# Performance work log

Measured on AMD Instinct MI355X. Metric: run time of the kernel, lower is better.

The kernel has to match this reference:

```python
import jax, jax.numpy as jnp
import numpy as np

EPS = 1e-8


def decode_fcos_obb(loc, deltas):
    """FCOS-style OBB decode. deltas = (d_x-, d_y-, d_z-, d_x+, d_y+, d_z+, theta):
    distances from the point to the 6 box faces, measured in the box's yaw-rotated
    frame. Returns OBB (x, y, z, w, l, h, theta)."""
    theta = deltas[:, 6]
    w = deltas[:, 0] + deltas[:, 3]
    l = deltas[:, 1] + deltas[:, 4]
    h = deltas[:, 2] + deltas[:, 5]
    ox = (deltas[:, 3] - deltas[:, 0]) * 0.5
    oy = (deltas[:, 4] - deltas[:, 1]) * 0.5
    oz = (deltas[:, 5] - deltas[:, 2]) * 0.5
    c, s = jnp.cos(theta), jnp.sin(theta)
    cx = loc[:, 0] + ox * c - oy * s
    cy = loc[:, 1] + ox * s + oy * c
    cz = loc[:, 2] + oz
    return jnp.stack([cx, cy, cz, w, l, h, theta], axis=-1)


def box2corners(box):
    # box: (B,N,5) = (x,y,w,h,alpha) -> (B,N,4,2) CCW corners
    x, y, w, h, a = (box[..., i] for i in range(5))
    x4 = jnp.asarray([0.5, -0.5, -0.5, 0.5], box.dtype) * w[..., None]
    y4 = jnp.asarray([0.5, 0.5, -0.5, -0.5], box.dtype) * h[..., None]
    c, s = jnp.cos(a)[..., None], jnp.sin(a)[..., None]
    return jnp.stack([x4 * c - y4 * s + x[..., None],
                      x4 * s + y4 * c + y[..., None]], axis=-1)


def box_intersection(corners1, corners2):
    # Pairwise intersections of the 4 edges of box1 with the 4 edges of box2.
    # Returns points (B,N,4,4,2) and validity mask (B,N,4,4).
    l1 = jnp.concatenate([corners1, jnp.roll(corners1, -1, axis=2)], axis=-1)[:, :, :, None, :]
    l2 = jnp.concatenate([corners2, jnp.roll(corners2, -1, axis=2)], axis=-1)[:, :, None, :, :]
    x1, y1, x2, y2 = l1[..., 0], l1[..., 1], l1[..., 2], l1[..., 3]
    x3, y3, x4, y4 = l2[..., 0], l2[..., 1], l2[..., 2], l2[..., 3]
    num = (y4 - y3) * (x2 - x1) - (x4 - x3) * (y2 - y1)
    den_t = (x4 - x3) * (y1 - y3) - (y4 - y3) * (x1 - x3)
    den_u = (x2 - x1) * (y1 - y3) - (y2 - y1) * (x1 - x3)
    safe = jnp.where(num == 0., 1., num)
    t = jnp.where(num == 0., -1., den_t / safe)
    u = jnp.where(num == 0., -1., -den_u / safe)
    mask = (t > 0.) & (t < 1.) & (u > 0.) & (u < 1.)
    t2 = den_t / (num + EPS)
    pts = jnp.stack([x1 + t2 * (x2 - x1), y1 + t2 * (y2 - y1)], axis=-1)
    pts = pts * mask[..., None].astype(pts.dtype)
    return pts, mask


def box1_in_box2(corners1, corners2):
    # Which corners of box1 lie inside box2 (projection onto box2's edge frame).
    a = corners2[:, :, 0:1, :]
    b = corners2[:, :, 1:2, :]
    d = corners2[:, :, 3:4, :]
    ab, ad, am = b - a, d - a, corners1 - a
    p_ab = (ab * am).sum(-1) / (ab * ab).sum(-1)
    p_ad = (ad * am).sum(-1) / (ad * ad).sum(-1)
    tol = 1e-6
    return (p_ab > -tol) & (p_ab < 1 + tol) & (p_ad > -tol) & (p_ad < 1 + tol)


def sorted_polygon_area(vertices, mask):
    # vertices: (B,N,24,2) candidate polygon vertices, mask: (B,N,24) validity.
    # Sort valid vertices CCW around their centroid, pad with the first vertex,
    # shoelace area. Equivalent to Rotated_IoU's sort_vertices + calculate_area.
    m = mask.astype(vertices.dtype)
    nv = m.sum(-1)  # (B,N) number of valid vertices
    mean = (vertices * m[..., None]).sum(2) / jnp.maximum(nv, 1.)[..., None]
    v = vertices - mean[:, :, None, :]
    ang = jnp.where(mask, jnp.arctan2(v[..., 1], v[..., 0]), 1e6)  # invalid -> last
    idx = jnp.argsort(ang, axis=-1)
    vs = jnp.take_along_axis(v, idx[..., None], axis=2)
    pos = jnp.arange(vertices.shape[2])
    pad = pos[None, None, :] >= nv[..., None]
    vs = jnp.where(pad[..., None], vs[:, :, :1, :], vs)  # pad with first valid vertex
    nxt = jnp.roll(vs, -1, axis=2)
    cross = vs[..., 0] * nxt[..., 1] - vs[..., 1] * nxt[..., 0]
    return 0.5 * jnp.abs(cross.sum(-1))


def cal_iou(box1, box2):
    c1 = box2corners(box1)
    c2 = box2corners(box2)
    pts, m_i = box_intersection(c1, c2)
    B, N = box1.shape[:2]
    vertices = jnp.concatenate([c1, c2, pts.reshape(B, N, 16, 2)], axis=2)
    mask = jnp.concatenate([box1_in_box2(c1, c2), box1_in_box2(c2, c1),
                            m_i.reshape(B, N, 16)], axis=2)
    inter = sorted_polygon_area(vertices, mask)
    u = box1[..., 2] * box1[..., 3] + box2[..., 2] * box2[..., 3] - inter
    return inter / u, u


def cal_iou_3d(b1, b2):
    # boxes: (B,N,7) = (x,y,z,w,l,h,theta); 2D rotated IoU in xy, overlap in z.
    box1 = jnp.stack([b1[..., 0], b1[..., 1], b1[..., 3], b1[..., 4], b1[..., 6]], -1)
    box2 = jnp.stack([b2[..., 0], b2[..., 1], b2[..., 3], b2[..., 4], b2[..., 6]], -1)
    zmax1, zmin1 = b1[..., 2] + b1[..., 5] * 0.5, b1[..., 2] - b1[..., 5] * 0.5
    zmax2, zmin2 = b2[..., 2] + b2[..., 5] * 0.5, b2[..., 2] - b2[..., 5] * 0.5
    z_overlap = jnp.clip(jnp.minimum(zmax1, zmax2) - jnp.maximum(zmin1, zmin2), 0.)
    iou_2d, u = cal_iou(box1, box2)
    inter_3d = iou_2d * u * z_overlap
    v1 = b1[..., 3] * b1[..., 4] * b1[..., 5]
    v2 = b2[..., 3] * b2[..., 4] * b2[..., 5]
    u3d = v1 + v2 - inter_3d
    return inter_3d / u3d, u3d


def rotated_iou_loss(pred, target, weight):
    loc = jnp.zeros((pred.shape[0], 3), pred.dtype)
    pb = decode_fcos_obb(loc, pred)[None]     # (1,N,7)
    tb = decode_fcos_obb(loc, target)[None]   # (1,N,7)
    ious, unions = cal_iou_3d(pb, tb)
    vol_inter = ious * unions
    ious = (vol_inter + 1.0) / (unions + 1.0)  # smoothed IoU
    losses = -jnp.log(ious)
    return (losses * weight).sum()


def setup_inputs():
    key = jax.random.key(0)
    k1, k2, k3 = jax.random.split(key, 3)
    N = 250000

    def make_deltas(k):
        u = jax.random.uniform(k, (N, 7), dtype=jnp.float32)
        dists = u[:, :6] * 2.0 + 0.3               # positive face distances
        theta = (u[:, 6:7] - 0.5) * jnp.pi          # yaw in (-pi/2, pi/2)
        return jnp.concatenate([dists, theta], axis=1)

    return {
        "pred": make_deltas(k1),
        "target": make_deltas(k2),
        "weight": jax.random.uniform(k3, (N,), dtype=jnp.float32),
    }


def reference(pred, target, weight):
    return rotated_iou_loss(pred, target, weight)
```

## Files before the change

kernel.cpp:

```cpp
#include <hip/hip_runtime.h>
#include <math.h>


#define RCP(x) __builtin_amdgcn_rcpf(x)

__global__ __launch_bounds__(256, 2) void riou_loss_kernel(
    const float* __restrict__ pred, const float* __restrict__ tgt,
    const float* __restrict__ wgt, float* __restrict__ ws, int n)
{
    int i = blockIdx.x * 256 + threadIdx.x;
    float loss = 0.0f;
    if (i < n) {
        const float* pp = pred + 7 * i;
        const float* qq = tgt + 7 * i;
        float p0 = pp[0], p1 = pp[1], p2 = pp[2], p3 = pp[3], p4 = pp[4], p5 = pp[5], p6 = pp[6];
        float q0 = qq[0], q1 = qq[1], q2 = qq[2], q3 = qq[3], q4 = qq[4], q5 = qq[5], q6 = qq[6];

        float w1 = p0 + p3, l1 = p1 + p4, h1 = p2 + p5;
        float oz1 = (p5 - p2) * 0.5f;
        float ox1 = (p3 - p0) * 0.5f, oy1 = (p4 - p1) * 0.5f;
        float sA = __sinf(p6), cA = __cosf(p6);
        float cx1 = ox1 * cA - oy1 * sA, cy1 = ox1 * sA + oy1 * cA;

        float w2 = q0 + q3, l2 = q1 + q4, h2 = q2 + q5;
        float oz2 = (q5 - q2) * 0.5f;
        float ox2 = (q3 - q0) * 0.5f, oy2 = (q4 - q1) * 0.5f;
        float sB = __sinf(q6), cB = __cosf(q6);
        float cx2 = ox2 * cB - oy2 * sB, cy2 = ox2 * sB + oy2 * cB;

        float vol1 = w1 * l1 * h1, vol2 = w2 * l2 * h2;
        float zo = fmaxf(fminf(oz1 + h1 * 0.5f, oz2 + h2 * 0.5f) -
                         fmaxf(oz1 - h1 * 0.5f, oz2 - h2 * 0.5f), 0.0f);

        float hw1 = 0.5f * w1, hl1 = 0.5f * l1;
        float c1x0 =  hw1 * cA - hl1 * sA + cx1, c1y0 =  hw1 * sA + hl1 * cA + cy1;
        float c1x1 = -hw1 * cA - hl1 * sA + cx1, c1y1 = -hw1 * sA + hl1 * cA + cy1;
        float c1x2 = -hw1 * cA + hl1 * sA + cx1, c1y2 = -hw1 * sA - hl1 * cA + cy1;
        float c1x3 =  hw1 * cA + hl1 * sA + cx1, c1y3 =  hw1 * sA - hl1 * cA + cy1;
        float hw2 = 0.5f * w2, hl2 = 0.5f * l2;
        float c2x0 =  hw2 * cB - hl2 * sB + cx2, c2y0 =  hw2 * sB + hl2 * cB + cy2;
        float c2x1 = -hw2 * cB - hl2 * sB + cx2, c2y1 = -hw2 * sB + hl2 * cB + cy2;
        float c2x2 = -hw2 * cB + hl2 * sB + cx2, c2y2 = -hw2 * sB - hl2 * cB + cy2;
        float c2x3 =  hw2 * cB + hl2 * sB + cx2, c2y3 =  hw2 * sB - hl2 * cB + cy2;

        float sumx = 0.0f, sumy = 0.0f;
        int nv = 0;
#define ACC(M, X, Y) { sumx += (M) ? (X) : 0.0f; sumy += (M) ? (Y) : 0.0f; nv += (M) ? 1 : 0; }

        const float TOL = 1e-6f;
        float abxB = c2x1 - c2x0, abyB = c2y1 - c2y0;
        float adxB = c2x3 - c2x0, adyB = c2y3 - c2y0;
        float rabB = RCP(abxB * abxB + abyB * abyB);
        float radB = RCP(adxB * adxB + adyB * adyB);
#define PIB_B(MX, MY, M) { float amx = (MX) - c2x0, amy = (MY) - c2y0; \
        float pab = (abxB * amx + abyB * amy) * rabB; \
        float pdd = (adxB * amx + adyB * amy) * radB; \
        M = (pab > -TOL) & (pab < 1.0f + TOL) & (pdd > -TOL) & (pdd < 1.0f + TOL); }
        bool mA0, mA1, mA2, mA3;
        PIB_B(c1x0, c1y0, mA0) PIB_B(c1x1, c1y1, mA1)
        PIB_B(c1x2, c1y2, mA2) PIB_B(c1x3, c1y3, mA3)
        ACC(mA0, c1x0, c1y0) ACC(mA1, c1x1, c1y1) ACC(mA2, c1x2, c1y2) ACC(mA3, c1x3, c1y3)
        float abxA = c1x1 - c1x0, abyA = c1y1 - c1y0;
        float adxA = c1x3 - c1x0, adyA = c1y3 - c1y0;
        float rabA = RCP(abxA * abxA + abyA * abyA);
        float radA = RCP(adxA * adxA + adyA * adyA);
#define PIB_A(MX, MY, M) { float amx = (MX) - c1x0, amy = (MY) - c1y0; \
        float pab = (abxA * amx + abyA * amy) * rabA; \
        float pdd = (adxA * amx + adyA * amy) * radA; \
        M = (pab > -TOL) & (pab < 1.0f + TOL) & (pdd > -TOL) & (pdd < 1.0f + TOL); }
        bool mB0, mB1, mB2, mB3;
        PIB_A(c2x0, c2y0, mB0) PIB_A(c2x1, c2y1, mB1)
        PIB_A(c2x2, c2y2, mB2) PIB_A(c2x3, c2y3, mB3)
        ACC(mB0, c2x0, c2y0) ACC(mB1, c2x1, c2y1) ACC(mB2, c2x2, c2y2) ACC(mB3, c2x3, c2y3)

#define ISECT(X1, Y1, X2, Y2, X3, Y3, X4, Y4, PX, PY, M) { \
        float ex = (X2) - (X1), ey = (Y2) - (Y1); \
        float fx = (X4) - (X3), fy = (Y4) - (Y3); \
        float gx = (X1) - (X3), gy = (Y1) - (Y3); \
        float num = fy * ex - fx * ey; \
        float dt_ = fx * gy - fy * gx; \
        float du_ = ex * gy - ey * gx; \
        float rr = RCP(num); \
        float tt = dt_ * rr, uu = -du_ * rr; \
        M = (tt > 0.0f) & (tt < 1.0f) & (uu > 0.0f) & (uu < 1.0f); \
        PX = (X1) + tt * ex; PY = (Y1) + tt * ey; }
#define SITEM(PX, PY, M, OX0, OY0, OX1, OY1, CNT) { \
        bool tk0 = (M) && ((CNT) == 0); bool tk1 = (M) && ((CNT) == 1); \
        OX0 = tk0 ? (PX) : OX0; OY0 = tk0 ? (PY) : OY0; \
        OX1 = tk1 ? (PX) : OX1; OY1 = tk1 ? (PY) : OY1; \
        CNT += (M) ? 1 : 0; }
#define EDGE_GROUP(X1, Y1, X2, Y2, EX0, EY0, EX1, EY1) { \
        int gc = 0; float px, py; bool mm; \
        ISECT(X1, Y1, X2, Y2, c2x0, c2y0, c2x1, c2y1, px, py, mm) \
        ACC(mm, px, py) SITEM(px, py, mm, EX0, EY0, EX1, EY1, gc) \
        ISECT(X1, Y1, X2, Y2, c2x1, c2y1, c2x2, c2y2, px, py, mm) \
        ACC(mm, px, py) SITEM(px, py, mm, EX0, EY0, EX1, EY1, gc) \
        ISECT(X1, Y1, X2, Y2, c2x2, c2y2, c2x3, c2y3, px, py, mm) \
        ACC(mm, px, py) SITEM(px, py, mm, EX0, EY0, EX1, EY1, gc) \
        ISECT(X1, Y1, X2, Y2, c2x3, c2y3, c2x0, c2y0, px, py, mm) \
        ACC(mm, px, py) SITEM(px, py, mm, EX0, EY0, EX1, EY1, gc) }

        float vx8 = 0.f, vy8 = 0.f, vx9 = 0.f, vy9 = 0.f;
        float vx10 = 0.f, vy10 = 0.f, vx11 = 0.f, vy11 = 0.f;
        float vx12 = 0.f, vy12 = 0.f, vx13 = 0.f, vy13 = 0.f;
        float vx14 = 0.f, vy14 = 0.f, vx15 = 0.f, vy15 = 0.f;
        int nv8_before = nv;
        EDGE_GROUP(c1x0, c1y0, c1x1, c1y1, vx8, vy8, vx9, vy9)
        int nv10_before = nv;
        EDGE_GROUP(c1x1, c1y1, c1x2, c1y2, vx10, vy10, vx11, vy11)
        int nv12_before = nv;
        EDGE_GROUP(c1x2, c1y2, c1x3, c1y3, vx12, vy12, vx13, vy13)
        int nv14_before = nv;
        EDGE_GROUP(c1x3, c1y3, c1x0, c1y0, vx14, vy14, vx15, vy15)
        bool m8  = (nv10_before - nv8_before) > 0, m9  = (nv10_before - nv8_before) > 1;
        bool m10 = (nv12_before - nv10_before) > 0, m11 = (nv12_before - nv10_before) > 1;
        bool m12 = (nv14_before - nv12_before) > 0, m13 = (nv14_before - nv12_before) > 1;
        bool m14 = (nv - nv14_before) > 0,          m15 = (nv - nv14_before) > 1;

        float vx0 = c1x0, vy0 = c1y0, vx1 = c1x1, vy1 = c1y1;
        float vx2 = c1x2, vy2 = c1y2, vx3 = c1x3, vy3 = c1y3;
        float vx4 = c2x0, vy4 = c2y0, vx5 = c2x1, vy5 = c2y1;
        float vx6 = c2x2, vy6 = c2y2, vx7 = c2x3, vy7 = c2y3;
        bool m0 = mA0, m1 = mA1, m2 = mA2, m3 = mA3;
        bool m4 = mB0, m5 = mB1, m6 = mB2, m7 = mB3;

        float inv_nv = RCP(fmaxf((float)nv, 1.0f));
        float mx_ = sumx * inv_nv, my_ = sumy * inv_nv;
        float ang0, ang1, ang2, ang3, ang4, ang5, ang6, ang7;
        float ang8, ang9, ang10, ang11, ang12, ang13, ang14, ang15;
        unsigned pk0, pk1, pk2, pk3, pk4, pk5, pk6, pk7;
        unsigned pk8, pk9, pk10, pk11, pk12, pk13, pk14, pk15;
#define ANGPACK(K) { float xc = vx##K - mx_, yc = vy##K - my_; \
        float dd = yc * RCP(fmaxf(fabsf(xc) + fabsf(yc), 1e-38f)); \
        ang##K = m##K ? ((xc >= 0.0f) ? dd : copysignf(2.0f, yc) - dd) : 1e6f; \
        pk##K = (__float_as_uint(xc) & 0xFFFF0000u) | (__float_as_uint(yc) >> 16); }
        ANGPACK(0) ANGPACK(1) ANGPACK(2) ANGPACK(3)
        ANGPACK(4) ANGPACK(5) ANGPACK(6) ANGPACK(7)
        ANGPACK(8) ANGPACK(9) ANGPACK(10) ANGPACK(11)
        ANGPACK(12) ANGPACK(13) ANGPACK(14) ANGPACK(15)

#define CE(A, B) { bool sw = ang##A > ang##B; \
        float mn = fminf(ang##A, ang##B), mx2 = fmaxf(ang##A, ang##B); \
        ang##A = mn; ang##B = mx2; \
        unsigned ta = pk##A; pk##A = sw ? pk##B : pk##A; pk##B = sw ? ta : pk##B; }
        CE(0,1) CE(2,3) CE(4,5) CE(6,7) CE(8,9) CE(10,11) CE(12,13) CE(14,15)
        CE(0,2) CE(1,3) CE(4,6) CE(5,7) CE(8,10) CE(9,11) CE(12,14) CE(13,15)
        CE(1,2) CE(5,6) CE(9,10) CE(13,14)
        CE(0,4) CE(1,5) CE(2,6) CE(3,7) CE(8,12) CE(9,13) CE(10,14) CE(11,15)
        CE(2,4) CE(3,5) CE(10,12) CE(11,13)
        CE(1,2) CE(3,4) CE(5,6) CE(9,10) CE(11,12) CE(13,14)
        CE(0,8) CE(1,9) CE(2,10) CE(3,11) CE(4,12) CE(5,13) CE(6,14) CE(7,15)
        CE(4,8) CE(5,9) CE(6,10) CE(7,11)
        CE(2,4) CE(3,5) CE(6,8) CE(7,9) CE(10,12) CE(11,13)
        CE(1,2) CE(3,4) CE(5,6) CE(7,8) CE(9,10) CE(11,12) CE(13,14)

#define PAD(K) { pk##K = (ang##K > 5e5f) ? pk0 : pk##K; }
        PAD(1) PAD(2) PAD(3) PAD(4) PAD(5) PAD(6) PAD(7) PAD(8)
        PAD(9) PAD(10) PAD(11) PAD(12) PAD(13) PAD(14) PAD(15)

#define UPX(K) float ux##K = __uint_as_float(pk##K & 0xFFFF0000u); \
               float uy##K = __uint_as_float(pk##K << 16);
        UPX(0) UPX(1) UPX(2) UPX(3) UPX(4) UPX(5) UPX(6) UPX(7)
        UPX(8) UPX(9) UPX(10) UPX(11) UPX(12) UPX(13) UPX(14) UPX(15)
        float cs = 0.0f;
#define SHOE(A, B) cs += ux##A * uy##B - uy##A * ux##B;
        SHOE(0,1) SHOE(1,2) SHOE(2,3) SHOE(3,4) SHOE(4,5) SHOE(5,6) SHOE(6,7) SHOE(7,8)
        SHOE(8,9) SHOE(9,10) SHOE(10,11) SHOE(11,12) SHOE(12,13) SHOE(13,14) SHOE(14,15) SHOE(15,0)
        float inter = 0.5f * fabsf(cs);

        float inter3d = inter * zo;
        float u3d = vol1 + vol2 - inter3d;
        float iouf = (inter3d + 1.0f) * RCP(u3d + 1.0f);
        loss = -__logf(iouf) * wgt[i];
    }

#pragma unroll
    for (int off = 32; off > 0; off >>= 1)
        loss += __shfl_down(loss, off, 64);
    __shared__ float wsum[4];
    int lane = threadIdx.x & 63, wid = threadIdx.x >> 6;
    if (lane == 0) wsum[wid] = loss;
    __syncthreads();
    if (threadIdx.x == 0)
        ws[blockIdx.x] = wsum[0] + wsum[1] + wsum[2] + wsum[3];
}

__global__ __launch_bounds__(256) void riou_reduce_kernel(
    const float* __restrict__ ws, float* __restrict__ out, int nb)
{
    float s = 0.0f;
    for (int t = threadIdx.x; t < nb; t += 256) s += ws[t];
#pragma unroll
    for (int off = 32; off > 0; off >>= 1)
        s += __shfl_down(s, off, 64);
    __shared__ float wsum[4];
    int lane = threadIdx.x & 63, wid = threadIdx.x >> 6;
    if (lane == 0) wsum[wid] = s;
    __syncthreads();
    if (threadIdx.x == 0)
        out[0] = wsum[0] + wsum[1] + wsum[2] + wsum[3];
}

extern "C" void kernel_launch(void* const* d_in, const int* in_sizes, int n_in,
                              void* d_out, int out_size, void* d_ws, size_t ws_size,
                              hipStream_t stream) {
    const float* pred = (const float*)d_in[0];
    const float* tgt  = (const float*)d_in[1];
    const float* wgt  = (const float*)d_in[2];
    float* out = (float*)d_out;
    float* ws  = (float*)d_ws;
    int n = in_sizes[2];

    int block = 256;
    int grid = (n + block - 1) / block;
    riou_loss_kernel<<<grid, block, 0, stream>>>(pred, tgt, wgt, ws, n);
    riou_reduce_kernel<<<1, block, 0, stream>>>(ws, out, grid);
}
```

Before: 77.06 us.

## Process two boxes per thread with paired float2-style arithmetic

Each thread now handles two elements (t and t+256) using a small f2 struct so the compiler can emit packed FP32 (v_pk_*) instructions on CDNA, and the grid is halved. Range checks are rewritten as |x-0.5|<0.5 forms, and the angle key uses a different pseudo-angle formula. Out-of-range elements are clamped and weighted by zero rather than branched. The risk is higher register pressure from doubled live state, which under launch_bounds(256,2) could cause spills or lower occupancy.

```diff
diff --git a/kernel.cpp b/kernel.cpp
--- a/kernel.cpp
+++ b/kernel.cpp
@@ -3,94 +3,139 @@
 
 
 #define RCP(x) __builtin_amdgcn_rcpf(x)
+
+struct f2 { float a, b; };
+struct b2 { bool a, b; };
+struct i2 { int a, b; };
+struct u2 { unsigned a, b; };
+
+__device__ __forceinline__ f2 operator+(f2 p, f2 q) { return {p.a + q.a, p.b + q.b}; }
+__device__ __forceinline__ f2 operator-(f2 p, f2 q) { return {p.a - q.a, p.b - q.b}; }
+__device__ __forceinline__ f2 operator*(f2 p, f2 q) { return {p.a * q.a, p.b * q.b}; }
+__device__ __forceinline__ f2 operator*(float s, f2 q) { return {s * q.a, s * q.b}; }
+__device__ __forceinline__ f2 operator-(f2 p) { return {-p.a, -p.b}; }
+__device__ __forceinline__ f2 rcp2(f2 p) { return {RCP(p.a), RCP(p.b)}; }
+__device__ __forceinline__ f2 fmin2(f2 p, f2 q) { return {fminf(p.a, q.a), fminf(p.b, q.b)}; }
+__device__ __forceinline__ f2 fmax2(f2 p, f2 q) { return {fmaxf(p.a, q.a), fmaxf(p.b, q.b)}; }
+__device__ __forceinline__ f2 fabs2(f2 p) { return {fabsf(p.a), fabsf(p.b)}; }
+__device__ __forceinline__ f2 cps2(f2 p, f2 s) { return {copysignf(p.a, s.a), copysignf(p.b, s.b)}; }
+__device__ __forceinline__ f2 sin2(f2 p) { return {__sinf(p.a), __sinf(p.b)}; }
+__device__ __forceinline__ f2 cos2(f2 p) { return {__cosf(p.a), __cosf(p.b)}; }
+__device__ __forceinline__ f2 log2f2(f2 p) { return {__logf(p.a), __logf(p.b)}; }
+__device__ __forceinline__ b2 lt2(f2 p, f2 q) { return {p.a < q.a, p.b < q.b}; }
+__device__ __forceinline__ b2 gt2(f2 p, f2 q) { return {p.a > q.a, p.b > q.b}; }
+__device__ __forceinline__ b2 and2(b2 p, b2 q) { return {p.a && q.a, p.b && q.b}; }
+__device__ __forceinline__ f2 sel(b2 c, f2 p, f2 q) { return {c.a ? p.a : q.a, c.b ? p.b : q.b}; }
+__device__ __forceinline__ u2 selu(b2 c, u2 p, u2 q) { return {c.a ? p.a : q.a, c.b ? p.b : q.b}; }
+__device__ __forceinline__ f2 i2f(i2 p) { return {(float)p.a, (float)p.b}; }
+
+__device__ __forceinline__ u2 pack2(f2 x, f2 y) {
+    return {(__float_as_uint(x.a) & 0xFFFF0000u) | (__float_as_uint(y.a) >> 16),
+            (__float_as_uint(x.b) & 0xFFFF0000u) | (__float_as_uint(y.b) >> 16)};
+}
+__device__ __forceinline__ f2 unpx(u2 p) {
+    return {__uint_as_float(p.a & 0xFFFF0000u), __uint_as_float(p.b & 0xFFFF0000u)};
+}
+__device__ __forceinline__ f2 unpy(u2 p) {
+    return {__uint_as_float(p.a << 16), __uint_as_float(p.b << 16)};
+}
 
 __global__ __launch_bounds__(256, 2) void riou_loss_kernel(
     const float* __restrict__ pred, const float* __restrict__ tgt,
     const float* __restrict__ wgt, float* __restrict__ ws, int n)
 {
-    int i = blockIdx.x * 256 + threadIdx.x;
-    float loss = 0.0f;
-    if (i < n) {
-        const float* pp = pred + 7 * i;
-        const float* qq = tgt + 7 * i;
-        float p0 = pp[0], p1 = pp[1], p2 = pp[2], p3 = pp[3], p4 = pp[4], p5 = pp[5], p6 = pp[6];
-        float q0 = qq[0], q1 = qq[1], q2 = qq[2], q3 = qq[3], q4 = qq[4], q5 = qq[5], q6 = qq[6];
-
-        float w1 = p0 + p3, l1 = p1 + p4, h1 = p2 + p5;
-        float oz1 = (p5 - p2) * 0.5f;
-        float ox1 = (p3 - p0) * 0.5f, oy1 = (p4 - p1) * 0.5f;
-        float sA = __sinf(p6), cA = __cosf(p6);
-        float cx1 = ox1 * cA - oy1 * sA, cy1 = ox1 * sA + oy1 * cA;
-
-        float w2 = q0 + q3, l2 = q1 + q4, h2 = q2 + q5;
-        float oz2 = (q5 - q2) * 0.5f;
-        float ox2 = (q3 - q0) * 0.5f, oy2 = (q4 - q1) * 0.5f;
-        float sB = __sinf(q6), cB = __cosf(q6);
-        float cx2 = ox2 * cB - oy2 * sB, cy2 = ox2 * sB + oy2 * cB;
-
-        float vol1 = w1 * l1 * h1, vol2 = w2 * l2 * h2;
-        float zo = fmaxf(fminf(oz1 + h1 * 0.5f, oz2 + h2 * 0.5f) -
-                         fmaxf(oz1 - h1 * 0.5f, oz2 - h2 * 0.5f), 0.0f);
-
-        float hw1 = 0.5f * w1, hl1 = 0.5f * l1;
-        float c1x0 =  hw1 * cA - hl1 * sA + cx1, c1y0 =  hw1 * sA + hl1 * cA + cy1;
-        float c1x1 = -hw1 * cA - hl1 * sA + cx1, c1y1 = -hw1 * sA + hl1 * cA + cy1;
-        float c1x2 = -hw1 * cA + hl1 * sA + cx1, c1y2 = -hw1 * sA - hl1 * cA + cy1;
-        float c1x3 =  hw1 * cA + hl1 * sA + cx1, c1y3 =  hw1 * sA - hl1 * cA + cy1;
-        float hw2 = 0.5f * w2, hl2 = 0.5f * l2;
-        float c2x0 =  hw2 * cB - hl2 * sB + cx2, c2y0 =  hw2 * sB + hl2 * cB + cy2;
-        float c2x1 = -hw2 * cB - hl2 * sB + cx2, c2y1 = -hw2 * sB + hl2 * cB + cy2;
-        float c2x2 = -hw2 * cB + hl2 * sB + cx2, c2y2 = -hw2 * sB - hl2 * cB + cy2;
-        float c2x3 =  hw2 * cB + hl2 * sB + cx2, c2y3 =  hw2 * sB - hl2 * cB + cy2;
-
-        float sumx = 0.0f, sumy = 0.0f;
-        int nv = 0;
-#define ACC(M, X, Y) { sumx += (M) ? (X) : 0.0f; sumy += (M) ? (Y) : 0.0f; nv += (M) ? 1 : 0; }
-
-        const float TOL = 1e-6f;
-        float abxB = c2x1 - c2x0, abyB = c2y1 - c2y0;
-        float adxB = c2x3 - c2x0, adyB = c2y3 - c2y0;
-        float rabB = RCP(abxB * abxB + abyB * abyB);
-        float radB = RCP(adxB * adxB + adyB * adyB);
-#define PIB_B(MX, MY, M) { float amx = (MX) - c2x0, amy = (MY) - c2y0; \
-        float pab = (abxB * amx + abyB * amy) * rabB; \
-        float pdd = (adxB * amx + adyB * amy) * radB; \
-        M = (pab > -TOL) & (pab < 1.0f + TOL) & (pdd > -TOL) & (pdd < 1.0f + TOL); }
-        bool mA0, mA1, mA2, mA3;
-        PIB_B(c1x0, c1y0, mA0) PIB_B(c1x1, c1y1, mA1)
-        PIB_B(c1x2, c1y2, mA2) PIB_B(c1x3, c1y3, mA3)
-        ACC(mA0, c1x0, c1y0) ACC(mA1, c1x1, c1y1) ACC(mA2, c1x2, c1y2) ACC(mA3, c1x3, c1y3)
-        float abxA = c1x1 - c1x0, abyA = c1y1 - c1y0;
-        float adxA = c1x3 - c1x0, adyA = c1y3 - c1y0;
-        float rabA = RCP(abxA * abxA + abyA * abyA);
-        float radA = RCP(adxA * adxA + adyA * adyA);
-#define PIB_A(MX, MY, M) { float amx = (MX) - c1x0, amy = (MY) - c1y0; \
-        float pab = (abxA * amx + abyA * amy) * rabA; \
-        float pdd = (adxA * amx + adyA * amy) * radA; \
-        M = (pab > -TOL) & (pab < 1.0f + TOL) & (pdd > -TOL) & (pdd < 1.0f + TOL); }
-        bool mB0, mB1, mB2, mB3;
-        PIB_A(c2x0, c2y0, mB0) PIB_A(c2x1, c2y1, mB1)
-        PIB_A(c2x2, c2y2, mB2) PIB_A(c2x3, c2y3, mB3)
-        ACC(mB0, c2x0, c2y0) ACC(mB1, c2x1, c2y1) ACC(mB2, c2x2, c2y2) ACC(mB3, c2x3, c2y3)
+    const f2 zero = {0.f, 0.f}, half = {0.5f, 0.5f}, onev = {1.f, 1.f};
+    const f2 bigv = {1e6f, 1e6f}, big5 = {5e5f, 5e5f}, tiny = {1e-38f, 1e-38f};
+    const f2 htv = {0.5f + 1e-6f, 0.5f + 1e-6f};
+
+    int t0 = blockIdx.x * 512 + threadIdx.x;
+    int t1 = t0 + 256;
+    int ia = min(t0, n - 1), ib = min(t1, n - 1);
+    f2 wg = {(t0 < n) ? wgt[ia] : 0.0f, (t1 < n) ? wgt[ib] : 0.0f};
+
+    const float* pA = pred + 7 * ia;  const float* pB = pred + 7 * ib;
+    const float* qA = tgt + 7 * ia;   const float* qB = tgt + 7 * ib;
+    f2 p0 = {pA[0], pB[0]}, p1 = {pA[1], pB[1]}, p2 = {pA[2], pB[2]}, p3 = {pA[3], pB[3]};
+    f2 p4 = {pA[4], pB[4]}, p5 = {pA[5], pB[5]}, p6 = {pA[6], pB[6]};
+    f2 q0 = {qA[0], qB[0]}, q1 = {qA[1], qB[1]}, q2 = {qA[2], qB[2]}, q3 = {qA[3], qB[3]};
+    f2 q4 = {qA[4], qB[4]}, q5 = {qA[5], qB[5]}, q6 = {qA[6], qB[6]};
+
+    f2 w1 = p0 + p3, l1 = p1 + p4, h1 = p2 + p5;
+    f2 oz1 = 0.5f * (p5 - p2);
+    f2 ox1 = 0.5f * (p3 - p0), oy1 = 0.5f * (p4 - p1);
+    f2 sA = sin2(p6), cA = cos2(p6);
+    f2 cx1 = ox1 * cA - oy1 * sA, cy1 = ox1 * sA + oy1 * cA;
+
+    f2 w2 = q0 + q3, l2 = q1 + q4, h2 = q2 + q5;
+    f2 oz2 = 0.5f * (q5 - q2);
+    f2 ox2 = 0.5f * (q3 - q0), oy2 = 0.5f * (q4 - q1);
+    f2 sB = sin2(q6), cB = cos2(q6);
+    f2 cx2 = ox2 * cB - oy2 * sB, cy2 = ox2 * sB + oy2 * cB;
+
+    f2 vol1 = w1 * l1 * h1, vol2 = w2 * l2 * h2;
+    f2 zo = fmax2(fmin2(oz1 + 0.5f * h1, oz2 + 0.5f * h2) -
+                  fmax2(oz1 - 0.5f * h1, oz2 - 0.5f * h2), zero);
+
+    f2 hw1 = 0.5f * w1, hl1 = 0.5f * l1;
+    f2 c1x0 = hw1 * cA - hl1 * sA + cx1, c1y0 = hw1 * sA + hl1 * cA + cy1;
+    f2 c1x1 = zero - hw1 * cA - hl1 * sA + cx1, c1y1 = zero - hw1 * sA + hl1 * cA + cy1;
+    f2 c1x2 = zero - hw1 * cA + hl1 * sA + cx1, c1y2 = zero - hw1 * sA - hl1 * cA + cy1;
+    f2 c1x3 = hw1 * cA + hl1 * sA + cx1, c1y3 = hw1 * sA - hl1 * cA + cy1;
+    f2 hw2 = 0.5f * w2, hl2 = 0.5f * l2;
+    f2 c2x0 = hw2 * cB - hl2 * sB + cx2, c2y0 = hw2 * sB + hl2 * cB + cy2;
+    f2 c2x1 = zero - hw2 * cB - hl2 * sB + cx2, c2y1 = zero - hw2 * sB + hl2 * cB + cy2;
+    f2 c2x2 = zero - hw2 * cB + hl2 * sB + cx2, c2y2 = zero - hw2 * sB - hl2 * cB + cy2;
+    f2 c2x3 = hw2 * cB + hl2 * sB + cx2, c2y3 = hw2 * sB - hl2 * cB + cy2;
+
+    f2 sumx = zero, sumy = zero;
+    i2 nv = {0, 0};
+#define ACC(M, X, Y) { sumx = sumx + sel(M, X, zero); sumy = sumy + sel(M, Y, zero); \
+        nv.a += (M).a; nv.b += (M).b; }
+
+    f2 abxB = c2x1 - c2x0, abyB = c2y1 - c2y0;
+    f2 adxB = c2x3 - c2x0, adyB = c2y3 - c2y0;
+    f2 rabB = rcp2(abxB * abxB + abyB * abyB);
+    f2 radB = rcp2(adxB * adxB + adyB * adyB);
+#define PIB_B(MX, MY, M) { f2 amx = (MX) - c2x0, amy = (MY) - c2y0; \
+        f2 pab = (abxB * amx + abyB * amy) * rabB; \
+        f2 pdd = (adxB * amx + adyB * amy) * radB; \
+        M = and2(lt2(fabs2(pab - half), htv), lt2(fabs2(pdd - half), htv)); }
+    b2 mA0, mA1, mA2, mA3;
+    PIB_B(c1x0, c1y0, mA0) PIB_B(c1x1, c1y1, mA1)
+    PIB_B(c1x2, c1y2, mA2) PIB_B(c1x3, c1y3, mA3)
+    ACC(mA0, c1x0, c1y0) ACC(mA1, c1x1, c1y1) ACC(mA2, c1x2, c1y2) ACC(mA3, c1x3, c1y3)
+    f2 abxA = c1x1 - c1x0, abyA = c1y1 - c1y0;
+    f2 adxA = c1x3 - c1x0, adyA = c1y3 - c1y0;
+    f2 rabA = rcp2(abxA * abxA + abyA * abyA);
+    f2 radA = rcp2(adxA * adxA + adyA * adyA);
+#define PIB_A(MX, MY, M) { f2 amx = (MX) - c1x0, amy = (MY) - c1y0; \
+        f2 pab = (abxA * amx + abyA * amy) * rabA; \
+        f2 pdd = (adxA * amx + adyA * amy) * radA; \
+        M = and2(lt2(fabs2(pab - half), htv), lt2(fabs2(pdd - half), htv)); }
+    b2 mB0, mB1, mB2, mB3;
+    PIB_A(c2x0, c2y0, mB0) PIB_A(c2x1, c2y1, mB1)
+    PIB_A(c2x2, c2y2, mB2) PIB_A(c2x3, c2y3, mB3)
+    ACC(mB0, c2x0, c2y0) ACC(mB1, c2x1, c2y1) ACC(mB2, c2x2, c2y2) ACC(mB3, c2x3, c2y3)
 
 #define ISECT(X1, Y1, X2, Y2, X3, Y3, X4, Y4, PX, PY, M) { \
-        float ex = (X2) - (X1), ey = (Y2) - (Y1); \
-        float fx = (X4) - (X3), fy = (Y4) - (Y3); \
-        float gx = (X1) - (X3), gy = (Y1) - (Y3); \
-        float num = fy * ex - fx * ey; \
-        float dt_ = fx * gy - fy * gx; \
-        float du_ = ex * gy - ey * gx; \
-        float rr = RCP(num); \
-        float tt = dt_ * rr, uu = -du_ * rr; \
-        M = (tt > 0.0f) & (tt < 1.0f) & (uu > 0.0f) & (uu < 1.0f); \
+        f2 ex = (X2) - (X1), ey = (Y2) - (Y1); \
+        f2 fx = (X4) - (X3), fy = (Y4) - (Y3); \
+        f2 gx = (X1) - (X3), gy = (Y1) - (Y3); \
+        f2 num = fy * ex - fx * ey; \
+        f2 dt_ = fx * gy - fy * gx; \
+        f2 du_ = ex * gy - ey * gx; \
+        f2 rr = rcp2(num); \
+        f2 tt = dt_ * rr, uu = zero - du_ * rr; \
+        M = and2(lt2(fabs2(tt - half), half), lt2(fabs2(uu - half), half)); \
         PX = (X1) + tt * ex; PY = (Y1) + tt * ey; }
 #define SITEM(PX, PY, M, OX0, OY0, OX1, OY1, CNT) { \
-        bool tk0 = (M) && ((CNT) == 0); bool tk1 = (M) && ((CNT) == 1); \
-        OX0 = tk0 ? (PX) : OX0; OY0 = tk0 ? (PY) : OY0; \
-        OX1 = tk1 ? (PX) : OX1; OY1 = tk1 ? (PY) : OY1; \
-        CNT += (M) ? 1 : 0; }
+        b2 tk0 = {(M).a && (CNT).a == 0, (M).b && (CNT).b == 0}; \
+        b2 tk1 = {(M).a && (CNT).a == 1, (M).b && (CNT).b == 1}; \
+        OX0 = sel(tk0, PX, OX0); OY0 = sel(tk0, PY, OY0); \
+        OX1 = sel(tk1, PX, OX1); OY1 = sel(tk1, PY, OY1); \
+        (CNT).a += (M).a; (CNT).b += (M).b; }
 #define EDGE_GROUP(X1, Y1, X2, Y2, EX0, EY0, EX1, EY1) { \
-        int gc = 0; float px, py; bool mm; \
+        i2 gc = {0, 0}; f2 px, py; b2 mm; \
         ISECT(X1, Y1, X2, Y2, c2x0, c2y0, c2x1, c2y1, px, py, mm) \
         ACC(mm, px, py) SITEM(px, py, mm, EX0, EY0, EX1, EY1, gc) \
         ISECT(X1, Y1, X2, Y2, c2x1, c2y1, c2x2, c2y2, px, py, mm) \
@@ -100,79 +145,83 @@
         ISECT(X1, Y1, X2, Y2, c2x3, c2y3, c2x0, c2y0, px, py, mm) \
         ACC(mm, px, py) SITEM(px, py, mm, EX0, EY0, EX1, EY1, gc) }
 
-        float vx8 = 0.f, vy8 = 0.f, vx9 = 0.f, vy9 = 0.f;
-        float vx10 = 0.f, vy10 = 0.f, vx11 = 0.f, vy11 = 0.f;
-        float vx12 = 0.f, vy12 = 0.f, vx13 = 0.f, vy13 = 0.f;
-        float vx14 = 0.f, vy14 = 0.f, vx15 = 0.f, vy15 = 0.f;
-        int nv8_before = nv;
-        EDGE_GROUP(c1x0, c1y0, c1x1, c1y1, vx8, vy8, vx9, vy9)
-        int nv10_before = nv;
-        EDGE_GROUP(c1x1, c1y1, c1x2, c1y2, vx10, vy10, vx11, vy11)
-        int nv12_before = nv;
-        EDGE_GROUP(c1x2, c1y2, c1x3, c1y3, vx12, vy12, vx13, vy13)
-        int nv14_before = nv;
-        EDGE_GROUP(c1x3, c1y3, c1x0, c1y0, vx14, vy14, vx15, vy15)
-        bool m8  = (nv10_before - nv8_before) > 0, m9  = (nv10_before - nv8_before) > 1;
-        bool m10 = (nv12_before - nv10_before) > 0, m11 = (nv12_before - nv10_before) > 1;
-        bool m12 = (nv14_before - nv12_before) > 0, m13 = (nv14_before - nv12_before) > 1;
-        bool m14 = (nv - nv14_before) > 0,          m15 = (nv - nv14_before) > 1;
-
-        float vx0 = c1x0, vy0 = c1y0, vx1 = c1x1, vy1 = c1y1;
-        float vx2 = c1x2, vy2 = c1y2, vx3 = c1x3, vy3 = c1y3;
-        float vx4 = c2x0, vy4 = c2y0, vx5 = c2x1, vy5 = c2y1;
-        float vx6 = c2x2, vy6 = c2y2, vx7 = c2x3, vy7 = c2y3;
-        bool m0 = mA0, m1 = mA1, m2 = mA2, m3 = mA3;
-        bool m4 = mB0, m5 = mB1, m6 = mB2, m7 = mB3;
-
-        float inv_nv = RCP(fmaxf((float)nv, 1.0f));
-        float mx_ = sumx * inv_nv, my_ = sumy * inv_nv;
-        float ang0, ang1, ang2, ang3, ang4, ang5, ang6, ang7;
-        float ang8, ang9, ang10, ang11, ang12, ang13, ang14, ang15;
-        unsigned pk0, pk1, pk2, pk3, pk4, pk5, pk6, pk7;
-        unsigned pk8, pk9, pk10, pk11, pk12, pk13, pk14, pk15;
-#define ANGPACK(K) { float xc = vx##K - mx_, yc = vy##K - my_; \
-        float dd = yc * RCP(fmaxf(fabsf(xc) + fabsf(yc), 1e-38f)); \
-        ang##K = m##K ? ((xc >= 0.0f) ? dd : copysignf(2.0f, yc) - dd) : 1e6f; \
-        pk##K = (__float_as_uint(xc) & 0xFFFF0000u) | (__float_as_uint(yc) >> 16); }
-        ANGPACK(0) ANGPACK(1) ANGPACK(2) ANGPACK(3)
-        ANGPACK(4) ANGPACK(5) ANGPACK(6) ANGPACK(7)
-        ANGPACK(8) ANGPACK(9) ANGPACK(10) ANGPACK(11)
-        ANGPACK(12) ANGPACK(13) ANGPACK(14) ANGPACK(15)
-
-#define CE(A, B) { bool sw = ang##A > ang##B; \
-        float mn = fminf(ang##A, ang##B), mx2 = fmaxf(ang##A, ang##B); \
+    f2 vx8 = zero, vy8 = zero, vx9 = zero, vy9 = zero;
+    f2 vx10 = zero, vy10 = zero, vx11 = zero, vy11 = zero;
+    f2 vx12 = zero, vy12 = zero, vx13 = zero, vy13 = zero;
+    f2 vx14 = zero, vy14 = zero, vx15 = zero, vy15 = zero;
+    i2 nv8b = nv;
+    EDGE_GROUP(c1x0, c1y0, c1x1, c1y1, vx8, vy8, vx9, vy9)
+    i2 nv10b = nv;
+    EDGE_GROUP(c1x1, c1y1, c1x2, c1y2, vx10, vy10, vx11, vy11)
+    i2 nv12b = nv;
+    EDGE_GROUP(c1x2, c1y2, c1x3, c1y3, vx12, vy12, vx13, vy13)
+    i2 nv14b = nv;
+    EDGE_GROUP(c1x3, c1y3, c1x0, c1y0, vx14, vy14, vx15, vy15)
+    b2 m8  = {nv10b.a - nv8b.a > 0, nv10b.b - nv8b.b > 0};
+    b2 m9  = {nv10b.a - nv8b.a > 1, nv10b.b - nv8b.b > 1};
+    b2 m10 = {nv12b.a - nv10b.a > 0, nv12b.b - nv10b.b > 0};
+    b2 m11 = {nv12b.a - nv10b.a > 1, nv12b.b - nv10b.b > 1};
+    b2 m12 = {nv14b.a - nv12b.a > 0, nv14b.b - nv12b.b > 0};
+    b2 m13 = {nv14b.a - nv12b.a > 1, nv14b.b - nv12b.b > 1};
+    b2 m14 = {nv.a - nv14b.a > 0, nv.b - nv14b.b > 0};
+    b2 m15 = {nv.a - nv14b.a > 1, nv.b - nv14b.b > 1};
+
+    f2 vx0 = c1x0, vy0 = c1y0, vx1 = c1x1, vy1 = c1y1;
+    f2 vx2 = c1x2, vy2 = c1y2, vx3 = c1x3, vy3 = c1y3;
+    f2 vx4 = c2x0, vy4 = c2y0, vx5 = c2x1, vy5 = c2y1;
+    f2 vx6 = c2x2, vy6 = c2y2, vx7 = c2x3, vy7 = c2y3;
+    b2 m0 = mA0, m1 = mA1, m2 = mA2, m3 = mA3;
+    b2 m4 = mB0, m5 = mB1, m6 = mB2, m7 = mB3;
+
+    f2 inv_nv = rcp2(fmax2(i2f(nv), onev));
+    f2 mx_ = sumx * inv_nv, my_ = sumy * inv_nv;
+    f2 ang0, ang1, ang2, ang3, ang4, ang5, ang6, ang7;
+    f2 ang8, ang9, ang10, ang11, ang12, ang13, ang14, ang15;
+    u2 pk0, pk1, pk2, pk3, pk4, pk5, pk6, pk7;
+    u2 pk8, pk9, pk10, pk11, pk12, pk13, pk14, pk15;
+#define ANGPACK(K) { f2 xc = vx##K - mx_, yc = vy##K - my_; \
+        f2 tt = xc * rcp2(fmax2(fabs2(xc) + fabs2(yc), tiny)); \
+        f2 key = cps2(onev - tt, yc); \
+        ang##K = sel(m##K, key, bigv); \
+        pk##K = pack2(xc, yc); }
+    ANGPACK(0) ANGPACK(1) ANGPACK(2) ANGPACK(3)
+    ANGPACK(4) ANGPACK(5) ANGPACK(6) ANGPACK(7)
+    ANGPACK(8) ANGPACK(9) ANGPACK(10) ANGPACK(11)
+    ANGPACK(12) ANGPACK(13) ANGPACK(14) ANGPACK(15)
+
+#define CE(A, B) { b2 sw = gt2(ang##A, ang##B); \
+        f2 mn = fmin2(ang##A, ang##B), mx2 = fmax2(ang##A, ang##B); \
         ang##A = mn; ang##B = mx2; \
-        unsigned ta = pk##A; pk##A = sw ? pk##B : pk##A; pk##B = sw ? ta : pk##B; }
-        CE(0,1) CE(2,3) CE(4,5) CE(6,7) CE(8,9) CE(10,11) CE(12,13) CE(14,15)
-        CE(0,2) CE(1,3) CE(4,6) CE(5,7) CE(8,10) CE(9,11) CE(12,14) CE(13,15)
-        CE(1,2) CE(5,6) CE(9,10) CE(13,14)
-        CE(0,4) CE(1,5) CE(2,6) CE(3,7) CE(8,12) CE(9,13) CE(10,14) CE(11,15)
-        CE(2,4) CE(3,5) CE(10,12) CE(11,13)
-        CE(1,2) CE(3,4) CE(5,6) CE(9,10) CE(11,12) CE(13,14)
-        CE(0,8) CE(1,9) CE(2,10) CE(3,11) CE(4,12) CE(5,13) CE(6,14) CE(7,15)
-        CE(4,8) CE(5,9) CE(6,10) CE(7,11)
-        CE(2,4) CE(3,5) CE(6,8) CE(7,9) CE(10,12) CE(11,13)
-        CE(1,2) CE(3,4) CE(5,6) CE(7,8) CE(9,10) CE(11,12) CE(13,14)
-
-#define PAD(K) { pk##K = (ang##K > 5e5f) ? pk0 : pk##K; }
-        PAD(1) PAD(2) PAD(3) PAD(4) PAD(5) PAD(6) PAD(7) PAD(8)
-        PAD(9) PAD(10) PAD(11) PAD(12) PAD(13) PAD(14) PAD(15)
-
-#define UPX(K) float ux##K = __uint_as_float(pk##K & 0xFFFF0000u); \
-               float uy##K = __uint_as_float(pk##K << 16);
-        UPX(0) UPX(1) UPX(2) UPX(3) UPX(4) UPX(5) UPX(6) UPX(7)
-        UPX(8) UPX(9) UPX(10) UPX(11) UPX(12) UPX(13) UPX(14) UPX(15)
-        float cs = 0.0f;
-#define SHOE(A, B) cs += ux##A * uy##B - uy##A * ux##B;
-        SHOE(0,1) SHOE(1,2) SHOE(2,3) SHOE(3,4) SHOE(4,5) SHOE(5,6) SHOE(6,7) SHOE(7,8)
-        SHOE(8,9) SHOE(9,10) SHOE(10,11) SHOE(11,12) SHOE(12,13) SHOE(13,14) SHOE(14,15) SHOE(15,0)
-        float inter = 0.5f * fabsf(cs);
-
-        float inter3d = inter * zo;
-        float u3d = vol1 + vol2 - inter3d;
-        float iouf = (inter3d + 1.0f) * RCP(u3d + 1.0f);
-        loss = -__logf(iouf) * wgt[i];
-    }
+        u2 ta = pk##A; pk##A = selu(sw, pk##B, pk##A); pk##B = selu(sw, ta, pk##B); }
+    CE(0,1) CE(2,3) CE(4,5) CE(6,7) CE(8,9) CE(10,11) CE(12,13) CE(14,15)
+    CE(0,2) CE(1,3) CE(4,6) CE(5,7) CE(8,10) CE(9,11) CE(12,14) CE(13,15)
+    CE(1,2) CE(5,6) CE(9,10) CE(13,14)
+    CE(0,4) CE(1,5) CE(2,6) CE(3,7) CE(8,12) CE(9,13) CE(10,14) CE(11,15)
+    CE(2,4) CE(3,5) CE(10,12) CE(11,13)
+    CE(1,2) CE(3,4) CE(5,6) CE(9,10) CE(11,12) CE(13,14)
+    CE(0,8) CE(1,9) CE(2,10) CE(3,11) CE(4,12) CE(5,13) CE(6,14) CE(7,15)
+    CE(4,8) CE(5,9) CE(6,10) CE(7,11)
+    CE(2,4) CE(3,5) CE(6,8) CE(7,9) CE(10,12) CE(11,13)
+    CE(1,2) CE(3,4) CE(5,6) CE(7,8) CE(9,10) CE(11,12) CE(13,14)
+
+#define PAD(K) { b2 pc = gt2(ang##K, big5); pk##K = selu(pc, pk0, pk##K); }
+    PAD(1) PAD(2) PAD(3) PAD(4) PAD(5) PAD(6) PAD(7) PAD(8)
+    PAD(9) PAD(10) PAD(11) PAD(12) PAD(13) PAD(14) PAD(15)
+
+#define UPX(K) f2 ux##K = unpx(pk##K); f2 uy##K = unpy(pk##K);
+    UPX(0) UPX(1) UPX(2) UPX(3) UPX(4) UPX(5) UPX(6) UPX(7)
+    UPX(8) UPX(9) UPX(10) UPX(11) UPX(12) UPX(13) UPX(14) UPX(15)
+    f2 cs = zero;
+#define SHOE(A, B) cs = cs + ux##A * uy##B - uy##A * ux##B;
+    SHOE(0,1) SHOE(1,2) SHOE(2,3) SHOE(3,4) SHOE(4,5) SHOE(5,6) SHOE(6,7) SHOE(7,8)
+    SHOE(8,9) SHOE(9,10) SHOE(10,11) SHOE(11,12) SHOE(12,13) SHOE(13,14) SHOE(14,15) SHOE(15,0)
+    f2 inter = 0.5f * fabs2(cs);
+
+    f2 inter3d = inter * zo;
+    f2 u3d = vol1 + vol2 - inter3d;
+    f2 iouf = (inter3d + onev) * rcp2(u3d + onev);
+    f2 lo2 = (zero - log2f2(iouf)) * wg;
+    float loss = lo2.a + lo2.b;
 
 #pragma unroll
     for (int off = 32; off > 0; off >>= 1)
@@ -211,8 +260,7 @@
     float* ws  = (float*)d_ws;
     int n = in_sizes[2];
 
-    int block = 256;
-    int grid = (n + block - 1) / block;
-    riou_loss_kernel<<<grid, block, 0, stream>>>(pred, tgt, wgt, ws, n);
-    riou_reduce_kernel<<<1, block, 0, stream>>>(ws, out, grid);
-}
+    int grid = (n + 511) / 512;
+    riou_loss_kernel<<<grid, 256, 0, stream>>>(pred, tgt, wgt, ws, n);
+    riou_reduce_kernel<<<1, 256, 0, stream>>>(ws, out, grid);
+}
```

After: 75.54 us. -2.0%, faster.
